# Kernel optimization log

Hardware: AMD Instinct MI355X
Metric: run time of the kernel (lower is better)

The kernel has to match this reference:

```python
import jax, jax.numpy as jnp
import numpy as np

SIGMA = 0.1
NUM_BINS = 256
EPS = 1e-10

def setup_inputs() -> dict:
    key = jax.random.key(0)
    k1, k2 = jax.random.split(key)
    B, C, H, W = 4, 1, 256, 256
    input1 = jax.random.uniform(k1, (B, C, H, W), dtype=jnp.float32)
    input2 = jax.random.uniform(k2, (B, C, H, W), dtype=jnp.float32)
    return {"input1": input1, "input2": input2}

def _kernel_and_marginal(x, bins):
    # x: (B, N, 1); bins: (NUM_BINS,)
    residuals = x - bins[None, None, :]                     # (B, N, NUM_BINS)
    kernel_values = jnp.exp(-0.5 * (residuals / SIGMA) ** 2)
    pdf = jnp.mean(kernel_values, axis=1)                   # (B, NUM_BINS)
    pdf = pdf / (jnp.sum(pdf, axis=1, keepdims=True) + EPS)
    return pdf, kernel_values

def reference(input1, input2):
    B, C, H, W = input1.shape
    x1 = (input1 * 255.0).reshape(B, H * W, C)              # C == 1
    x2 = (input2 * 255.0).reshape(B, H * W, C)
    bins = jnp.linspace(0.0, 255.0, NUM_BINS, dtype=jnp.float32)

    pdf_x1, kv1 = _kernel_and_marginal(x1, bins)
    pdf_x2, kv2 = _kernel_and_marginal(x2, bins)

    # joint histogram: (B, NUM_BINS, N) @ (B, N, NUM_BINS)
    joint = jnp.einsum('bni,bnj->bij', kv1, kv2)
    joint = joint / (jnp.sum(joint, axis=(1, 2), keepdims=True) + EPS)

    H_x1 = -jnp.sum(pdf_x1 * jnp.log2(pdf_x1 + EPS), axis=1)
    H_x2 = -jnp.sum(pdf_x2 * jnp.log2(pdf_x2 + EPS), axis=1)
    H_x1x2 = -jnp.sum(joint * jnp.log2(joint + EPS), axis=(1, 2))

    mi = H_x1 + H_x2 - H_x1x2
    mi = 2.0 * mi / (H_x1 + H_x2)  # normalize=True
    return jnp.mean(mi)
```

## Files before the change

### kernel.cpp

```cpp
#include <hip/hip_runtime.h>

#define NBINS  256
#define BATCH  4
#define NPIX   65536
#define EPSF   1e-10f
#define RSTRIP 16
#define NSTRIP 16
#define NQ     4
#define QPIX   (NPIX / NQ)

__global__ __launch_bounds__(1024) void mi_strip(
    const float* __restrict__ in1, const float* __restrict__ in2,
    float* __restrict__ S1part, float* __restrict__ S2part,
    float* __restrict__ Jpart)
{
    __shared__ float js[RSTRIP * NBINS];
    __shared__ float h1[NBINS];
    __shared__ float h2[NBINS];

    const int t  = threadIdx.x;
    const int b  = blockIdx.x >> 6;
    const int s  = (blockIdx.x >> 2) & (NSTRIP - 1);
    const int q  = blockIdx.x & (NQ - 1);
    const int r0 = s << 4;

#pragma unroll
    for (int i = 0; i < 4; ++i) js[(i << 10) + t] = 0.0f;
    if (t < NBINS) { h1[t] = 0.0f; h2[t] = 0.0f; }
    __syncthreads();

    const float4* __restrict__ p1 = (const float4*)(in1 + b * NPIX) + q * (QPIX / 4);
    const float4* __restrict__ p2 = (const float4*)(in2 + b * NPIX) + q * (QPIX / 4);

#pragma unroll
    for (int it = 0; it < QPIX / 4096; ++it) {
        const int l = (it << 10) + t;
        const float4 a = p1[l];
        const float4 c = p2[l];
        const bool mflag = (l >> 8) == s;

        const float vx1[4] = { a.x, a.y, a.z, a.w };
        const float vx2[4] = { c.x, c.y, c.z, c.w };
#pragma unroll
        for (int j = 0; j < 4; ++j) {
            const float v1 = vx1[j] * 255.0f;
            const float v2 = vx2[j] * 255.0f;
            const int k1 = (int)v1;
            const int k2 = (int)v2;
            const float d1 = v1 - (float)k1;
            const float d2 = v2 - (float)k2;
            const float e1 = d1 - 1.0f;
            const float e2 = d2 - 1.0f;
            const float w1a = __expf(-50.0f * d1 * d1);
            const float w1b = __expf(-50.0f * e1 * e1);
            const float w2a = __expf(-50.0f * d2 * d2);
            const float w2b = __expf(-50.0f * e2 * e2);

            const int r = k1 - r0;
            if ((unsigned)r < RSTRIP) {
                atomicAdd(&js[(r << 8) + k2],     w1a * w2a);
                atomicAdd(&js[(r << 8) + k2 + 1], w1a * w2b);
            }
            if ((unsigned)(r + 1) < RSTRIP) {
                atomicAdd(&js[((r + 1) << 8) + k2],     w1b * w2a);
                atomicAdd(&js[((r + 1) << 8) + k2 + 1], w1b * w2b);
            }
            if (mflag) {
                atomicAdd(&h1[k1],     w1a);
                atomicAdd(&h1[k1 + 1], w1b);
                atomicAdd(&h2[k2],     w2a);
                atomicAdd(&h2[k2 + 1], w2b);
            }
        }
    }
    __syncthreads();

    float* __restrict__ Jq = Jpart + ((size_t)(b * NQ + q) << 16) + (r0 << 8);
#pragma unroll
    for (int i = 0; i < 4; ++i) {
        const int idx = (i << 10) + t;
        Jq[idx] = js[idx];
    }
    if (t < NBINS) {
        const size_t po = (size_t)(((b * NSTRIP + s) * NQ + q)) << 8;
        S1part[po + t] = h1[t];
        S2part[po + t] = h2[t];
    }
}

__global__ __launch_bounds__(1024) void mi_entrop(
    const float* __restrict__ Jpart, float* __restrict__ SJ, float* __restrict__ TJ)
{
    __shared__ float red[1024];
    const int t   = threadIdx.x;
    const int b   = blockIdx.x >> 2;
    const int g   = blockIdx.x & 3;
    const int col = t & (NBINS - 1);
    const int ro  = t >> 8;
    const float* __restrict__ J0 = Jpart + ((size_t)(b * NQ) << 16);

    float Sacc = 0.0f, Tacc = 0.0f;
#pragma unroll 4
    for (int k = 0; k < 16; ++k) {
        const int row = (g << 6) + (ro << 4) + k;
        const size_t off = ((size_t)row << 8) + col;
        const float c = J0[off] + J0[off + (1 << 16)]
                      + J0[off + (2 << 16)] + J0[off + (3 << 16)];
        Sacc += c;
        Tacc += (c > 1e-30f) ? c * __log2f(c) : 0.0f;
    }
    red[t] = Sacc; __syncthreads();
    for (int s = 512; s > 0; s >>= 1) { if (t < s) red[t] += red[t + s]; __syncthreads(); }
    const float Stot = red[0]; __syncthreads();
    red[t] = Tacc; __syncthreads();
    for (int s = 512; s > 0; s >>= 1) { if (t < s) red[t] += red[t + s]; __syncthreads(); }
    if (t == 0) { SJ[blockIdx.x] = Stot; TJ[blockIdx.x] = red[0]; }
}

__global__ __launch_bounds__(1024) void mi_combine(
    const float* __restrict__ S1part, const float* __restrict__ S2part,
    const float* __restrict__ SJ, const float* __restrict__ TJ,
    float* __restrict__ out)
{
    __shared__ float red[1024];
    __shared__ float nmi[BATCH];
    const int t   = threadIdx.x;
    const int b   = t >> 8;
    const int bin = t & (NBINS - 1);
    const float invN = 1.0f / (float)NPIX;

    const float* __restrict__ q1 = S1part + ((size_t)b << 14) + bin;
    const float* __restrict__ q2 = S2part + ((size_t)b << 14) + bin;
    float a1 = 0.0f, a2 = 0.0f;
#pragma unroll 8
    for (int j = 0; j < 64; ++j) { a1 += q1[(size_t)j << 8]; a2 += q2[(size_t)j << 8]; }
    const float pre1 = a1 * invN;
    const float pre2 = a2 * invN;

    auto segreduce = [&](float v) -> float {
        red[t] = v; __syncthreads();
        for (int s = 128; s > 0; s >>= 1) {
            if (bin < s) red[t] += red[t + s];
            __syncthreads();
        }
        const float r = red[b << 8];
        __syncthreads();
        return r;
    };

    const float sum1 = segreduce(pre1);
    const float p1 = pre1 / (sum1 + EPSF);
    const float H1 = segreduce(-p1 * __log2f(p1 + EPSF));

    const float sum2 = segreduce(pre2);
    const float p2 = pre2 / (sum2 + EPSF);
    const float H2 = segreduce(-p2 * __log2f(p2 + EPSF));

    const float SJb = SJ[b << 2] + SJ[(b << 2) + 1] + SJ[(b << 2) + 2] + SJ[(b << 2) + 3];
    const float TJb = TJ[b << 2] + TJ[(b << 2) + 1] + TJ[(b << 2) + 2] + TJ[(b << 2) + 3];
    const float Sp  = SJb + EPSF;
    const float H12 = __log2f(Sp) * (SJb / Sp) - TJb / Sp;

    if (bin == 0) {
        const float mi = H1 + H2 - H12;
        nmi[b] = 2.0f * mi / (H1 + H2);
    }
    __syncthreads();
    if (t == 0) *out = 0.25f * (nmi[0] + nmi[1] + nmi[2] + nmi[3]);
}

extern "C" void kernel_launch(void* const* d_in, const int* in_sizes, int n_in,
                              void* d_out, int out_size, void* d_ws, size_t ws_size,
                              hipStream_t stream)
{
    const float* in1 = (const float*)d_in[0];
    const float* in2 = (const float*)d_in[1];

    float* S1part = (float*)d_ws;
    float* S2part = S1part + BATCH * NSTRIP * NQ * NBINS;
    float* Jpart  = S2part + BATCH * NSTRIP * NQ * NBINS;
    float* SJ     = Jpart + (size_t)BATCH * NQ * NBINS * NBINS;
    float* TJ     = SJ + BATCH * NQ;
    float* out    = (float*)d_out;

    mi_strip<<<BATCH * NSTRIP * NQ, 1024, 0, stream>>>(in1, in2, S1part, S2part, Jpart);
    mi_entrop<<<BATCH * NQ, 1024, 0, stream>>>(Jpart, SJ, TJ);
    mi_combine<<<1, 1024, 0, stream>>>(S1part, S2part, SJ, TJ, out);
}
```

Baseline: 35.81 us.

## Fuse three kernels into one cooperative kernel with grid syncs

Replaces the strip, entropy and combine kernels with a single cooperative launch of 256 blocks that uses two grid-wide syncs between phases. The joint-histogram reduction is redistributed so all 256 blocks each reduce a 16x64 tile with wave shuffles, instead of 16 blocks doing large tree reductions. Marginal partials also get a two-level reduction. This removes two kernel launch gaps and makes the reduction phases more parallel. In exchange it adds grid-sync cost and requires all 256 blocks of 1024 threads to be co-resident.

```diff
diff --git a/kernel.cpp b/kernel.cpp
--- a/kernel.cpp
+++ b/kernel.cpp
@@ -1,4 +1,7 @@
 #include <hip/hip_runtime.h>
+#include <hip/hip_cooperative_groups.h>
+
+namespace cg = cooperative_groups;
 
 #define NBINS  256
 #define BATCH  4
@@ -9,164 +12,173 @@
 #define NQ     4
 #define QPIX   (NPIX / NQ)
 
-__global__ __launch_bounds__(1024) void mi_strip(
+__global__ __launch_bounds__(1024) void mi_fused(
     const float* __restrict__ in1, const float* __restrict__ in2,
-    float* __restrict__ S1part, float* __restrict__ S2part,
-    float* __restrict__ Jpart)
+    float* __restrict__ Jpart,
+    float* __restrict__ M1q, float* __restrict__ M2q,
+    float* __restrict__ M1m, float* __restrict__ M2m,
+    float* __restrict__ STs, float* __restrict__ STt,
+    float* __restrict__ out)
 {
     __shared__ float js[RSTRIP * NBINS];
     __shared__ float h1[NBINS];
     __shared__ float h2[NBINS];
-
-    const int t  = threadIdx.x;
-    const int b  = blockIdx.x >> 6;
-    const int s  = (blockIdx.x >> 2) & (NSTRIP - 1);
-    const int q  = blockIdx.x & (NQ - 1);
-    const int r0 = s << 4;
-
-#pragma unroll
-    for (int i = 0; i < 4; ++i) js[(i << 10) + t] = 0.0f;
-    if (t < NBINS) { h1[t] = 0.0f; h2[t] = 0.0f; }
-    __syncthreads();
-
-    const float4* __restrict__ p1 = (const float4*)(in1 + b * NPIX) + q * (QPIX / 4);
-    const float4* __restrict__ p2 = (const float4*)(in2 + b * NPIX) + q * (QPIX / 4);
-
-#pragma unroll
-    for (int it = 0; it < QPIX / 4096; ++it) {
-        const int l = (it << 10) + t;
-        const float4 a = p1[l];
-        const float4 c = p2[l];
-        const bool mflag = (l >> 8) == s;
-
-        const float vx1[4] = { a.x, a.y, a.z, a.w };
-        const float vx2[4] = { c.x, c.y, c.z, c.w };
-#pragma unroll
-        for (int j = 0; j < 4; ++j) {
-            const float v1 = vx1[j] * 255.0f;
-            const float v2 = vx2[j] * 255.0f;
-            const int k1 = (int)v1;
-            const int k2 = (int)v2;
-            const float d1 = v1 - (float)k1;
-            const float d2 = v2 - (float)k2;
-            const float e1 = d1 - 1.0f;
-            const float e2 = d2 - 1.0f;
-            const float w1a = __expf(-50.0f * d1 * d1);
-            const float w1b = __expf(-50.0f * e1 * e1);
-            const float w2a = __expf(-50.0f * d2 * d2);
-            const float w2b = __expf(-50.0f * e2 * e2);
-
-            const int r = k1 - r0;
-            if ((unsigned)r < RSTRIP) {
-                atomicAdd(&js[(r << 8) + k2],     w1a * w2a);
-                atomicAdd(&js[(r << 8) + k2 + 1], w1a * w2b);
+    __shared__ float red[1024];
+    __shared__ float sb[BATCH], tb[BATCH], nmiS[BATCH];
+
+    const int t   = threadIdx.x;
+    const int blk = blockIdx.x;
+
+    {
+        const int b  = blk >> 6;
+        const int s  = (blk >> 2) & (NSTRIP - 1);
+        const int q  = blk & (NQ - 1);
+        const int r0 = s << 4;
+
+#pragma unroll
+        for (int i = 0; i < 4; ++i) js[(i << 10) + t] = 0.0f;
+        if (t < NBINS) { h1[t] = 0.0f; h2[t] = 0.0f; }
+        __syncthreads();
+
+        const float4* __restrict__ p1 = (const float4*)(in1 + b * NPIX) + q * (QPIX / 4);
+        const float4* __restrict__ p2 = (const float4*)(in2 + b * NPIX) + q * (QPIX / 4);
+
+#pragma unroll
+        for (int it = 0; it < QPIX / 4096; ++it) {
+            const int l = (it << 10) + t;
+            const float4 a = p1[l];
+            const float4 c = p2[l];
+            const bool mflag = (l >> 8) == s;
+
+            const float vx1[4] = { a.x, a.y, a.z, a.w };
+            const float vx2[4] = { c.x, c.y, c.z, c.w };
+#pragma unroll
+            for (int j = 0; j < 4; ++j) {
+                const float v1 = vx1[j] * 255.0f;
+                const float v2 = vx2[j] * 255.0f;
+                const int k1 = (int)v1;
+                const int k2 = (int)v2;
+                const float d1 = v1 - (float)k1;
+                const float d2 = v2 - (float)k2;
+                const float e1 = d1 - 1.0f;
+                const float e2 = d2 - 1.0f;
+                const float w1a = __expf(-50.0f * d1 * d1);
+                const float w1b = __expf(-50.0f * e1 * e1);
+                const float w2a = __expf(-50.0f * d2 * d2);
+                const float w2b = __expf(-50.0f * e2 * e2);
+
+                const int r = k1 - r0;
+                if ((unsigned)r < RSTRIP) {
+                    atomicAdd(&js[(r << 8) + k2],     w1a * w2a);
+                    atomicAdd(&js[(r << 8) + k2 + 1], w1a * w2b);
+                }
+                if ((unsigned)(r + 1) < RSTRIP) {
+                    atomicAdd(&js[((r + 1) << 8) + k2],     w1b * w2a);
+                    atomicAdd(&js[((r + 1) << 8) + k2 + 1], w1b * w2b);
+                }
+                if (mflag) {
+                    atomicAdd(&h1[k1],     w1a);
+                    atomicAdd(&h1[k1 + 1], w1b);
+                    atomicAdd(&h2[k2],     w2a);
+                    atomicAdd(&h2[k2 + 1], w2b);
+                }
             }
-            if ((unsigned)(r + 1) < RSTRIP) {
-                atomicAdd(&js[((r + 1) << 8) + k2],     w1b * w2a);
-                atomicAdd(&js[((r + 1) << 8) + k2 + 1], w1b * w2b);
+        }
+        __syncthreads();
+
+        float* __restrict__ Jq = Jpart + ((size_t)blk << 12);
+#pragma unroll
+        for (int i = 0; i < 4; ++i) { const int idx = (i << 10) + t; Jq[idx] = js[idx]; }
+        if (t < NBINS) {
+            M1q[(blk << 8) + t] = h1[t];
+            M2q[(blk << 8) + t] = h2[t];
+        }
+    }
+
+    cg::this_grid().sync();
+
+    {
+        const int g    = blk >> 2;
+        const int cgrp = blk & 3;
+        const int ri   = t >> 6;
+        const int col  = (cgrp << 6) + (t & 63);
+        const size_t ci = ((size_t)ri << 8) + col;
+        const float* __restrict__ J0 = Jpart + ((size_t)(g << 2) << 12);
+
+        const float c = J0[ci] + J0[ci + 4096] + J0[ci + 8192] + J0[ci + 12288];
+        float S = c;
+        float T = (c > 1e-30f) ? c * __log2f(c) : 0.0f;
+#pragma unroll
+        for (int m = 32; m >= 1; m >>= 1) { S += __shfl_xor(S, m); T += __shfl_xor(T, m); }
+        const int wid = t >> 6, lane = t & 63;
+        if (lane == 0) { red[wid] = S; red[32 + wid] = T; }
+
+        if (cgrp == 0 && t < 512) {
+            const int arr = t >> 8, bin = t & 255;
+            const float* __restrict__ Mq = (arr == 0 ? M1q : M2q) + (g << 10) + bin;
+            const float mv = Mq[0] + Mq[256] + Mq[512] + Mq[768];
+            if (arr == 0) M1m[(g << 8) + bin] = mv;
+            else          M2m[(g << 8) + bin] = mv;
+        }
+        __syncthreads();
+        if (t == 0) {
+            float ss = 0.0f, tt = 0.0f;
+#pragma unroll
+            for (int w = 0; w < 16; ++w) { ss += red[w]; tt += red[32 + w]; }
+            STs[blk] = ss; STt[blk] = tt;
+        }
+    }
+
+    cg::this_grid().sync();
+
+    if (blk == 0) {
+        const int wid = t >> 6, lane = t & 63;
+        if (wid < BATCH) {
+            float S = STs[(wid << 6) + lane];
+            float T = STt[(wid << 6) + lane];
+#pragma unroll
+            for (int m = 32; m >= 1; m >>= 1) { S += __shfl_xor(S, m); T += __shfl_xor(T, m); }
+            if (lane == 0) { sb[wid] = S; tb[wid] = T; }
+        }
+        __syncthreads();
+
+        const int b = t >> 8, bin = t & 255;
+        const float invN = 1.0f / (float)NPIX;
+        const float* __restrict__ q1 = M1m + ((size_t)b << 12) + bin;
+        const float* __restrict__ q2 = M2m + ((size_t)b << 12) + bin;
+        float a1 = 0.0f, a2 = 0.0f;
+#pragma unroll
+        for (int s = 0; s < 16; ++s) { a1 += q1[s << 8]; a2 += q2[s << 8]; }
+        const float pre1 = a1 * invN, pre2 = a2 * invN;
+
+        auto segreduce = [&](float v) -> float {
+            red[t] = v; __syncthreads();
+            for (int s = 128; s > 0; s >>= 1) {
+                if (bin < s) red[t] += red[t + s];
+                __syncthreads();
             }
-            if (mflag) {
-                atomicAdd(&h1[k1],     w1a);
-                atomicAdd(&h1[k1 + 1], w1b);
-                atomicAdd(&h2[k2],     w2a);
-                atomicAdd(&h2[k2 + 1], w2b);
-            }
-        }
+            const float r = red[b << 8];
+            __syncthreads();
+            return r;
+        };
+
+        const float sum1 = segreduce(pre1);
+        const float p1 = pre1 / (sum1 + EPSF);
+        const float H1 = segreduce(-p1 * __log2f(p1 + EPSF));
+
+        const float sum2 = segreduce(pre2);
+        const float p2 = pre2 / (sum2 + EPSF);
+        const float H2 = segreduce(-p2 * __log2f(p2 + EPSF));
+
+        if (bin == 0) {
+            const float Sp  = sb[b] + EPSF;
+            const float H12 = __log2f(Sp) * (sb[b] / Sp) - tb[b] / Sp;
+            const float mi  = H1 + H2 - H12;
+            nmiS[b] = 2.0f * mi / (H1 + H2);
+        }
+        __syncthreads();
+        if (t == 0) *out = 0.25f * (nmiS[0] + nmiS[1] + nmiS[2] + nmiS[3]);
     }
-    __syncthreads();
-
-    float* __restrict__ Jq = Jpart + ((size_t)(b * NQ + q) << 16) + (r0 << 8);
-#pragma unroll
-    for (int i = 0; i < 4; ++i) {
-        const int idx = (i << 10) + t;
-        Jq[idx] = js[idx];
-    }
-    if (t < NBINS) {
-        const size_t po = (size_t)(((b * NSTRIP + s) * NQ + q)) << 8;
-        S1part[po + t] = h1[t];
-        S2part[po + t] = h2[t];
-    }
-}
-
-__global__ __launch_bounds__(1024) void mi_entrop(
-    const float* __restrict__ Jpart, float* __restrict__ SJ, float* __restrict__ TJ)
-{
-    __shared__ float red[1024];
-    const int t   = threadIdx.x;
-    const int b   = blockIdx.x >> 2;
-    const int g   = blockIdx.x & 3;
-    const int col = t & (NBINS - 1);
-    const int ro  = t >> 8;
-    const float* __restrict__ J0 = Jpart + ((size_t)(b * NQ) << 16);
-
-    float Sacc = 0.0f, Tacc = 0.0f;
-#pragma unroll 4
-    for (int k = 0; k < 16; ++k) {
-        const int row = (g << 6) + (ro << 4) + k;
-        const size_t off = ((size_t)row << 8) + col;
-        const float c = J0[off] + J0[off + (1 << 16)]
-                      + J0[off + (2 << 16)] + J0[off + (3 << 16)];
-        Sacc += c;
-        Tacc += (c > 1e-30f) ? c * __log2f(c) : 0.0f;
-    }
-    red[t] = Sacc; __syncthreads();
-    for (int s = 512; s > 0; s >>= 1) { if (t < s) red[t] += red[t + s]; __syncthreads(); }
-    const float Stot = red[0]; __syncthreads();
-    red[t] = Tacc; __syncthreads();
-    for (int s = 512; s > 0; s >>= 1) { if (t < s) red[t] += red[t + s]; __syncthreads(); }
-    if (t == 0) { SJ[blockIdx.x] = Stot; TJ[blockIdx.x] = red[0]; }
-}
-
-__global__ __launch_bounds__(1024) void mi_combine(
-    const float* __restrict__ S1part, const float* __restrict__ S2part,
-    const float* __restrict__ SJ, const float* __restrict__ TJ,
-    float* __restrict__ out)
-{
-    __shared__ float red[1024];
-    __shared__ float nmi[BATCH];
-    const int t   = threadIdx.x;
-    const int b   = t >> 8;
-    const int bin = t & (NBINS - 1);
-    const float invN = 1.0f / (float)NPIX;
-
-    const float* __restrict__ q1 = S1part + ((size_t)b << 14) + bin;
-    const float* __restrict__ q2 = S2part + ((size_t)b << 14) + bin;
-    float a1 = 0.0f, a2 = 0.0f;
-#pragma unroll 8
-    for (int j = 0; j < 64; ++j) { a1 += q1[(size_t)j << 8]; a2 += q2[(size_t)j << 8]; }
-    const float pre1 = a1 * invN;
-    const float pre2 = a2 * invN;
-
-    auto segreduce = [&](float v) -> float {
-        red[t] = v; __syncthreads();
-        for (int s = 128; s > 0; s >>= 1) {
-            if (bin < s) red[t] += red[t + s];
-            __syncthreads();
-        }
-        const float r = red[b << 8];
-        __syncthreads();
-        return r;
-    };
-
-    const float sum1 = segreduce(pre1);
-    const float p1 = pre1 / (sum1 + EPSF);
-    const float H1 = segreduce(-p1 * __log2f(p1 + EPSF));
-
-    const float sum2 = segreduce(pre2);
-    const float p2 = pre2 / (sum2 + EPSF);
-    const float H2 = segreduce(-p2 * __log2f(p2 + EPSF));
-
-    const float SJb = SJ[b << 2] + SJ[(b << 2) + 1] + SJ[(b << 2) + 2] + SJ[(b << 2) + 3];
-    const float TJb = TJ[b << 2] + TJ[(b << 2) + 1] + TJ[(b << 2) + 2] + TJ[(b << 2) + 3];
-    const float Sp  = SJb + EPSF;
-    const float H12 = __log2f(Sp) * (SJb / Sp) - TJb / Sp;
-
-    if (bin == 0) {
-        const float mi = H1 + H2 - H12;
-        nmi[b] = 2.0f * mi / (H1 + H2);
-    }
-    __syncthreads();
-    if (t == 0) *out = 0.25f * (nmi[0] + nmi[1] + nmi[2] + nmi[3]);
 }
 
 extern "C" void kernel_launch(void* const* d_in, const int* in_sizes, int n_in,
@@ -176,14 +188,17 @@
     const float* in1 = (const float*)d_in[0];
     const float* in2 = (const float*)d_in[1];
 
-    float* S1part = (float*)d_ws;
-    float* S2part = S1part + BATCH * NSTRIP * NQ * NBINS;
-    float* Jpart  = S2part + BATCH * NSTRIP * NQ * NBINS;
-    float* SJ     = Jpart + (size_t)BATCH * NQ * NBINS * NBINS;
-    float* TJ     = SJ + BATCH * NQ;
-    float* out    = (float*)d_out;
-
-    mi_strip<<<BATCH * NSTRIP * NQ, 1024, 0, stream>>>(in1, in2, S1part, S2part, Jpart);
-    mi_entrop<<<BATCH * NQ, 1024, 0, stream>>>(Jpart, SJ, TJ);
-    mi_combine<<<1, 1024, 0, stream>>>(S1part, S2part, SJ, TJ, out);
+    float* Jpart = (float*)d_ws;
+    float* M1q   = Jpart + (size_t)256 * 4096;
+    float* M2q   = M1q + 65536;
+    float* M1m   = M2q + 65536;
+    float* M2m   = M1m + 16384;
+    float* STs   = M2m + 16384;
+    float* STt   = STs + 256;
+    float* outp  = (float*)d_out;
+
+    void* args[] = { (void*)&in1, (void*)&in2, (void*)&Jpart, (void*)&M1q, (void*)&M2q,
+                     (void*)&M1m, (void*)&M2m, (void*)&STs, (void*)&STt, (void*)&outp };
+    (void)hipLaunchCooperativeKernel((const void*)mi_fused, dim3(256), dim3(1024),
+                                     args, 0, stream);
 }
```

Result: slower. 96.93 us (+170.7%).

## Fuse entropy and combine kernels via last-block ticket, widen entropy grid

Applied to the files above, without the earlier changes.

Merges the final combine kernel into the entropy kernel using global atomics and a ticket counter, so the last finishing block computes the output. This removes one kernel launch. The entropy grid also grows from 16 to 256 blocks, one element per thread, with wavefront shuffle reductions replacing the shared-memory tree, to spread the Jpart read over more CUs. Accumulators are reset in the first kernel, which makes correctness depend on stream ordering and on atomic float sums, whose order is not deterministic.

```diff
diff --git a/kernel.cpp b/kernel.cpp
--- a/kernel.cpp
+++ b/kernel.cpp
@@ -12,7 +12,9 @@
 __global__ __launch_bounds__(1024) void mi_strip(
     const float* __restrict__ in1, const float* __restrict__ in2,
     float* __restrict__ S1part, float* __restrict__ S2part,
-    float* __restrict__ Jpart)
+    float* __restrict__ Jpart,
+    float* __restrict__ accS, float* __restrict__ accT,
+    unsigned* __restrict__ ticket)
 {
     __shared__ float js[RSTRIP * NBINS];
     __shared__ float h1[NBINS];
@@ -23,6 +25,12 @@
     const int s  = (blockIdx.x >> 2) & (NSTRIP - 1);
     const int q  = blockIdx.x & (NQ - 1);
     const int r0 = s << 4;
+
+    if (blockIdx.x == 0 && t == 0) {
+        *ticket = 0u;
+#pragma unroll
+        for (int i = 0; i < BATCH; ++i) { accS[i] = 0.0f; accT[i] = 0.0f; }
+    }
 
 #pragma unroll
     for (int i = 0; i < 4; ++i) js[(i << 10) + t] = 0.0f;
@@ -77,73 +85,75 @@
 
     float* __restrict__ Jq = Jpart + ((size_t)(b * NQ + q) << 16) + (r0 << 8);
 #pragma unroll
-    for (int i = 0; i < 4; ++i) {
-        const int idx = (i << 10) + t;
-        Jq[idx] = js[idx];
-    }
+    for (int i = 0; i < 4; ++i) { const int idx = (i << 10) + t; Jq[idx] = js[idx]; }
     if (t < NBINS) {
-        const size_t po = (size_t)(((b * NSTRIP + s) * NQ + q)) << 8;
+        const size_t po = (size_t)((b * NSTRIP + s) * NQ + q) << 8;
         S1part[po + t] = h1[t];
         S2part[po + t] = h2[t];
     }
 }
 
 __global__ __launch_bounds__(1024) void mi_entrop(
-    const float* __restrict__ Jpart, float* __restrict__ SJ, float* __restrict__ TJ)
+    const float* __restrict__ Jpart,
+    const float* __restrict__ S1part, const float* __restrict__ S2part,
+    float* __restrict__ accS, float* __restrict__ accT,
+    unsigned* __restrict__ ticket, float* __restrict__ out)
 {
     __shared__ float red[1024];
+    __shared__ float sb[BATCH], tb[BATCH], nmiS[BATCH];
+    __shared__ unsigned tickS;
+
     const int t   = threadIdx.x;
-    const int b   = blockIdx.x >> 2;
-    const int g   = blockIdx.x & 3;
+    const int g   = blockIdx.x;
+    const int b   = g >> 6;
+    const int row = ((g & 63) << 2) + (t >> 8);
     const int col = t & (NBINS - 1);
-    const int ro  = t >> 8;
+    const size_t off = ((size_t)row << 8) + col;
     const float* __restrict__ J0 = Jpart + ((size_t)(b * NQ) << 16);
 
-    float Sacc = 0.0f, Tacc = 0.0f;
-#pragma unroll 4
-    for (int k = 0; k < 16; ++k) {
-        const int row = (g << 6) + (ro << 4) + k;
-        const size_t off = ((size_t)row << 8) + col;
-        const float c = J0[off] + J0[off + (1 << 16)]
-                      + J0[off + (2 << 16)] + J0[off + (3 << 16)];
-        Sacc += c;
-        Tacc += (c > 1e-30f) ? c * __log2f(c) : 0.0f;
+    const float c = J0[off] + J0[off + (1 << 16)]
+                  + J0[off + (2 << 16)] + J0[off + (3 << 16)];
+    float S = c;
+    float T = (c > 1e-30f) ? c * __log2f(c) : 0.0f;
+#pragma unroll
+    for (int m = 32; m >= 1; m >>= 1) { S += __shfl_xor(S, m); T += __shfl_xor(T, m); }
+    const int wid = t >> 6, lane = t & 63;
+    if (lane == 0) { red[wid] = S; red[16 + wid] = T; }
+    __syncthreads();
+    if (t == 0) {
+        float ss = 0.0f, tt = 0.0f;
+#pragma unroll
+        for (int w = 0; w < 16; ++w) { ss += red[w]; tt += red[16 + w]; }
+        const float oldS = atomicAdd(&accS[b], ss);
+        const float oldT = atomicAdd(&accT[b], tt);
+        asm volatile("" :: "v"(oldS), "v"(oldT));
+        tickS = atomicAdd(ticket, 1u);
     }
-    red[t] = Sacc; __syncthreads();
-    for (int s = 512; s > 0; s >>= 1) { if (t < s) red[t] += red[t + s]; __syncthreads(); }
-    const float Stot = red[0]; __syncthreads();
-    red[t] = Tacc; __syncthreads();
-    for (int s = 512; s > 0; s >>= 1) { if (t < s) red[t] += red[t + s]; __syncthreads(); }
-    if (t == 0) { SJ[blockIdx.x] = Stot; TJ[blockIdx.x] = red[0]; }
-}
+    __syncthreads();
+    if (tickS != 255u) return;
 
-__global__ __launch_bounds__(1024) void mi_combine(
-    const float* __restrict__ S1part, const float* __restrict__ S2part,
-    const float* __restrict__ SJ, const float* __restrict__ TJ,
-    float* __restrict__ out)
-{
-    __shared__ float red[1024];
-    __shared__ float nmi[BATCH];
-    const int t   = threadIdx.x;
-    const int b   = t >> 8;
-    const int bin = t & (NBINS - 1);
+    if (t < BATCH) {
+        sb[t] = atomicAdd(&accS[t], 0.0f);
+        tb[t] = atomicAdd(&accT[t], 0.0f);
+    }
+    __syncthreads();
+
+    const int bb = t >> 8, bin = t & (NBINS - 1);
     const float invN = 1.0f / (float)NPIX;
-
-    const float* __restrict__ q1 = S1part + ((size_t)b << 14) + bin;
-    const float* __restrict__ q2 = S2part + ((size_t)b << 14) + bin;
+    const float* __restrict__ q1 = S1part + ((size_t)bb << 14) + bin;
+    const float* __restrict__ q2 = S2part + ((size_t)bb << 14) + bin;
     float a1 = 0.0f, a2 = 0.0f;
 #pragma unroll 8
     for (int j = 0; j < 64; ++j) { a1 += q1[(size_t)j << 8]; a2 += q2[(size_t)j << 8]; }
-    const float pre1 = a1 * invN;
-    const float pre2 = a2 * invN;
+    const float pre1 = a1 * invN, pre2 = a2 * invN;
 
     auto segreduce = [&](float v) -> float {
         red[t] = v; __syncthreads();
-        for (int s = 128; s > 0; s >>= 1) {
-            if (bin < s) red[t] += red[t + s];
+        for (int st = 128; st > 0; st >>= 1) {
+            if (bin < st) red[t] += red[t + st];
             __syncthreads();
         }
-        const float r = red[b << 8];
+        const float r = red[bb << 8];
         __syncthreads();
         return r;
     };
@@ -156,17 +166,14 @@
     const float p2 = pre2 / (sum2 + EPSF);
     const float H2 = segreduce(-p2 * __log2f(p2 + EPSF));
 
-    const float SJb = SJ[b << 2] + SJ[(b << 2) + 1] + SJ[(b << 2) + 2] + SJ[(b << 2) + 3];
-    const float TJb = TJ[b << 2] + TJ[(b << 2) + 1] + TJ[(b << 2) + 2] + TJ[(b << 2) + 3];
-    const float Sp  = SJb + EPSF;
-    const float H12 = __log2f(Sp) * (SJb / Sp) - TJb / Sp;
-
     if (bin == 0) {
-        const float mi = H1 + H2 - H12;
-        nmi[b] = 2.0f * mi / (H1 + H2);
+        const float Sp  = sb[bb] + EPSF;
+        const float H12 = __log2f(Sp) * (sb[bb] / Sp) - tb[bb] / Sp;
+        const float mi  = H1 + H2 - H12;
+        nmiS[bb] = 2.0f * mi / (H1 + H2);
     }
     __syncthreads();
-    if (t == 0) *out = 0.25f * (nmi[0] + nmi[1] + nmi[2] + nmi[3]);
+    if (t == 0) *out = 0.25f * (nmiS[0] + nmiS[1] + nmiS[2] + nmiS[3]);
 }
 
 extern "C" void kernel_launch(void* const* d_in, const int* in_sizes, int n_in,
@@ -176,14 +183,16 @@
     const float* in1 = (const float*)d_in[0];
     const float* in2 = (const float*)d_in[1];
 
-    float* S1part = (float*)d_ws;
-    float* S2part = S1part + BATCH * NSTRIP * NQ * NBINS;
-    float* Jpart  = S2part + BATCH * NSTRIP * NQ * NBINS;
-    float* SJ     = Jpart + (size_t)BATCH * NQ * NBINS * NBINS;
-    float* TJ     = SJ + BATCH * NQ;
-    float* out    = (float*)d_out;
+    float*    S1part = (float*)d_ws;
+    float*    S2part = S1part + BATCH * NSTRIP * NQ * NBINS;
+    float*    Jpart  = S2part + BATCH * NSTRIP * NQ * NBINS;
+    float*    accS   = Jpart + (size_t)BATCH * NQ * NBINS * NBINS;
+    float*    accT   = accS + BATCH;
+    unsigned* ticket = (unsigned*)(accT + BATCH);
+    float*    outp   = (float*)d_out;
 
-    mi_strip<<<BATCH * NSTRIP * NQ, 1024, 0, stream>>>(in1, in2, S1part, S2part, Jpart);
-    mi_entrop<<<BATCH * NQ, 1024, 0, stream>>>(Jpart, SJ, TJ);
-    mi_combine<<<1, 1024, 0, stream>>>(S1part, S2part, SJ, TJ, out);
+    mi_strip<<<BATCH * NSTRIP * NQ, 1024, 0, stream>>>(
+        in1, in2, S1part, S2part, Jpart, accS, accT, ticket);
+    mi_entrop<<<256, 1024, 0, stream>>>(
+        Jpart, S1part, S2part, accS, accT, ticket, outp);
 }
```

New measurement: 41.25 us. 1.15x slower.
